# Kernel tuning notes

Hardware: AMD Instinct MI355X
Metric: run time of the kernel (lower is better)

The kernel has to match this reference:

```python
import jax, jax.numpy as jnp
import numpy as np

N_NODES = 50000
N_EDGES = 600000
D = 128
R = 8


def setup_inputs() -> dict:
    key = jax.random.key(0)
    ks = jax.random.split(key, 10)
    return {
        "node_ids": jnp.arange(N_NODES, dtype=jnp.int32),
        "src": jax.random.randint(ks[0], (N_EDGES,), 0, N_NODES, dtype=jnp.int32),
        "dst": jax.random.randint(ks[1], (N_EDGES,), 0, N_NODES, dtype=jnp.int32),
        "etype": jax.random.randint(ks[2], (N_EDGES,), 0, R, dtype=jnp.int32),
        "emb": jax.random.normal(ks[3], (N_NODES, D), dtype=jnp.float32) * 0.02,
        "W1": jax.random.normal(ks[4], (R, D, D), dtype=jnp.float32) * 0.05,
        "Wself1": jax.random.normal(ks[5], (D, D), dtype=jnp.float32) * 0.05,
        "b1": jnp.zeros((D,), dtype=jnp.float32),
        "W2": jax.random.normal(ks[6], (R, D, D), dtype=jnp.float32) * 0.05,
        "Wself2": jax.random.normal(ks[7], (D, D), dtype=jnp.float32) * 0.05,
        "b2": jnp.zeros((D,), dtype=jnp.float32),
    }


def rgcn_layer(h, W, Wself, b, src, dst, etype, n_nodes):
    # relation-wise transform of all node features: [R, N, d_out]
    hr = jnp.einsum('nd,rdo->rno', h, W)
    # per-edge gather of (relation, src) -> message, then scatter-sum to dst
    msgs = hr[etype, src]                                   # [E, d_out]
    agg = jax.ops.segment_sum(msgs, dst, num_segments=n_nodes)
    # self-loop + bias (activation=None, feat_drop=0)
    return agg + h @ Wself + b


def reference(node_ids, src, dst, etype, emb, W1, Wself1, b1, W2, Wself2, b2):
    h0 = emb[node_ids]                                      # embedding lookup over all nodes
    h1 = rgcn_layer(h0, W1, Wself1, b1, src, dst, etype, emb.shape[0])
    h2 = rgcn_layer(h1, W2, Wself2, b2, src, dst, etype, emb.shape[0])
    return h2
```

## Files before the change

kernel.cpp:

```cpp
#include <hip/hip_runtime.h>
#include <hip/hip_bf16.h>

#define NN 50000
#define NE 600000
#define DD 128
#define NR 8
#define NCHUNK ((NN + 255) / 256)

typedef __attribute__((ext_vector_type(8))) short bf16x8;
typedef __attribute__((ext_vector_type(4))) float f32x4;

__device__ __forceinline__ unsigned short f2bf(float f) {
  __hip_bfloat16 h = __float2bfloat16(f);
  return *reinterpret_cast<unsigned short*>(&h);
}
__device__ __forceinline__ unsigned pk2(float lo, float hi) {
  return (unsigned)f2bf(lo) | ((unsigned)f2bf(hi) << 16);
}
__device__ __forceinline__ float bflo(unsigned u) { return __uint_as_float(u << 16); }
__device__ __forceinline__ float bfhi(unsigned u) { return __uint_as_float(u & 0xffff0000u); }

__global__ __launch_bounds__(128) void convw_kernel(
    const float* __restrict__ W1, const float* __restrict__ Ws1,
    const float* __restrict__ W2, const float* __restrict__ Ws2,
    unsigned short* __restrict__ WT)
{
  const int m = blockIdx.y, o = blockIdx.x, d = threadIdx.x;
  const float* src;
  if (m < 8)       src = W1 + (size_t)m * DD * DD;
  else if (m == 8) src = Ws1;
  else if (m < 17) src = W2 + (size_t)(m - 9) * DD * DD;
  else             src = Ws2;
  WT[(size_t)m * DD * DD + o * DD + d] = f2bf(src[(size_t)d * DD + o]);
}

template<int AF32, int OUTF32>
__global__ __launch_bounds__(256) void transform_mfma(
    const void* __restrict__ hin, const int* __restrict__ ids,
    const unsigned short* __restrict__ WT,
    const float* __restrict__ bias,
    unsigned short* __restrict__ hr,
    void* __restrict__ outSelf)
{
  __shared__ __align__(16) char ldsW[DD * DD * 2];

  const int r = blockIdx.y;
  const int rowBase = blockIdx.x * 64;
  const int tid = threadIdx.x;

  {
    const unsigned short* wsrc = WT + (size_t)r * DD * DD;
#pragma unroll
    for (int j = 0; j < 8; ++j) {
      const int i = tid + j * 256;
      const int o = i >> 4, seg = i & 15;
      uint4 v = *reinterpret_cast<const uint4*>(wsrc + o * DD + seg * 8);
      const int dstB = ((o << 8) + (seg << 4)) ^ ((o & 7) << 4);
      *reinterpret_cast<uint4*>(ldsW + dstB) = v;
    }
  }

  const int lane = tid & 63;
  const int w = tid >> 6;
  const int c = lane & 15;
  const int g = lane >> 4;
  const int n = rowBase + w * 16 + c;
  const int nld = (n < NN) ? n : (NN - 1);

  bf16x8 hfrag[4];
  if (AF32) {
    const int srcRow = ids[nld];
    const float* hrow = (const float*)hin + (size_t)srcRow * DD;
#pragma unroll
    for (int ks = 0; ks < 4; ++ks) {
      const float4 x = *reinterpret_cast<const float4*>(hrow + ks * 32 + g * 8);
      const float4 y = *reinterpret_cast<const float4*>(hrow + ks * 32 + g * 8 + 4);
      uint4 u;
      u.x = pk2(x.x, x.y); u.y = pk2(x.z, x.w);
      u.z = pk2(y.x, y.y); u.w = pk2(y.z, y.w);
      hfrag[ks] = *reinterpret_cast<bf16x8*>(&u);
    }
  } else {
    const unsigned short* hrow = (const unsigned short*)hin + (size_t)nld * DD;
#pragma unroll
    for (int ks = 0; ks < 4; ++ks) {
      uint4 u = *reinterpret_cast<const uint4*>(hrow + ks * 32 + g * 8);
      hfrag[ks] = *reinterpret_cast<bf16x8*>(&u);
    }
  }

  __syncthreads();

  f32x4 acc[8];
#pragma unroll
  for (int t = 0; t < 8; ++t) acc[t] = (f32x4){0.f, 0.f, 0.f, 0.f};

#pragma unroll
  for (int ks = 0; ks < 4; ++ks) {
#pragma unroll
    for (int t = 0; t < 8; ++t) {
      const int addr = (((t * 16 + c) << 8) + (ks << 6) + (g << 4)) ^ ((c & 7) << 4);
      bf16x8 a = *reinterpret_cast<const bf16x8*>(ldsW + addr);
      acc[t] = __builtin_amdgcn_mfma_f32_16x16x32_bf16(a, hfrag[ks], acc[t], 0, 0, 0);
    }
  }

  if (n >= NN) return;

  if (r < NR) {
    unsigned short* dst = hr + ((size_t)r * NN + n) * DD;
#pragma unroll
    for (int t = 0; t < 8; ++t) {
      const int o0 = t * 16 + g * 4;
      uint2 u;
      u.x = pk2(acc[t][0], acc[t][1]);
      u.y = pk2(acc[t][2], acc[t][3]);
      *reinterpret_cast<uint2*>(dst + o0) = u;
    }
  } else if (OUTF32) {
    float* dst = (float*)outSelf + (size_t)n * DD;
#pragma unroll
    for (int t = 0; t < 8; ++t) {
      const int o0 = t * 16 + g * 4;
      const float4 bv = *reinterpret_cast<const float4*>(bias + o0);
      float4 o;
      o.x = acc[t][0] + bv.x; o.y = acc[t][1] + bv.y;
      o.z = acc[t][2] + bv.z; o.w = acc[t][3] + bv.w;
      *reinterpret_cast<float4*>(dst + o0) = o;
    }
  } else {
    unsigned short* dst = (unsigned short*)outSelf + (size_t)n * DD;
#pragma unroll
    for (int t = 0; t < 8; ++t) {
      const int o0 = t * 16 + g * 4;
      const float4 bv = *reinterpret_cast<const float4*>(bias + o0);
      uint2 u;
      u.x = pk2(acc[t][0] + bv.x, acc[t][1] + bv.y);
      u.y = pk2(acc[t][2] + bv.z, acc[t][3] + bv.w);
      *reinterpret_cast<uint2*>(dst + o0) = u;
    }
  }
}

__global__ __launch_bounds__(256) void hist_kernel(
    const int* __restrict__ dst, int* __restrict__ deg)
{
  const int e = blockIdx.x * 256 + threadIdx.x;
  if (e < NE) atomicAdd(&deg[dst[e]], 1);
}

__global__ __launch_bounds__(256) void bsum_kernel(
    const int* __restrict__ deg, int* __restrict__ bsum)
{
  __shared__ int tmp[256];
  const int t = threadIdx.x;
  const int i = blockIdx.x * 256 + t;
  tmp[t] = (i < NN) ? deg[i] : 0;
  __syncthreads();
#pragma unroll
  for (int off = 128; off > 0; off >>= 1) {
    if (t < off) tmp[t] += tmp[t + off];
    __syncthreads();
  }
  if (t == 0) bsum[blockIdx.x] = tmp[0];
}

__global__ __launch_bounds__(256) void bscan_kernel(
    const int* __restrict__ bsum, int* __restrict__ bbase)
{
  __shared__ int tmp[256];
  const int t = threadIdx.x;
  const int v = (t < NCHUNK) ? bsum[t] : 0;
  tmp[t] = v;
  __syncthreads();
#pragma unroll
  for (int off = 1; off < 256; off <<= 1) {
    const int x = (t >= off) ? tmp[t - off] : 0;
    __syncthreads();
    tmp[t] += x;
    __syncthreads();
  }
  if (t < NCHUNK) bbase[t] = tmp[t] - v;
}

__global__ __launch_bounds__(256) void expand_kernel(
    int* deg, const int* __restrict__ bbase, int* __restrict__ offsets)
{
  __shared__ int tmp[256];
  const int t = threadIdx.x;
  const int i = blockIdx.x * 256 + t;
  const int v = (i < NN) ? deg[i] : 0;
  tmp[t] = v;
  __syncthreads();
#pragma unroll
  for (int off = 1; off < 256; off <<= 1) {
    const int x = (t >= off) ? tmp[t - off] : 0;
    __syncthreads();
    tmp[t] += x;
    __syncthreads();
  }
  const int base = bbase[blockIdx.x];
  const int excl = base + tmp[t] - v;
  if (i < NN) {
    offsets[i] = excl;
    deg[i] = excl;
    if (i == NN - 1) offsets[NN] = base + tmp[t];
  }
}

__global__ __launch_bounds__(256) void fill_kernel(
    const int* __restrict__ src, const int* __restrict__ dst,
    const int* __restrict__ et, int* __restrict__ cursor,
    int* __restrict__ eidx)
{
  const int e = blockIdx.x * 256 + threadIdx.x;
  if (e < NE) {
    const int pos = atomicAdd(&cursor[dst[e]], 1);
    eidx[pos] = et[e] * NN + src[e];
  }
}

template<int BF16OUT>
__global__ __launch_bounds__(256) void aggregate_kernel(
    const unsigned short* __restrict__ hr,
    const int* __restrict__ offsets, const int* __restrict__ eidx,
    void* __restrict__ outv)
{
  const int node = blockIdx.x * 4 + (threadIdx.x >> 6);
  const int lane = threadIdx.x & 63;
  if (node >= NN) return;
  const int beg = offsets[node];
  const int end = offsets[node + 1];

  float a0 = 0.f, a1 = 0.f;
  int e = beg;
  for (; e + 3 < end; e += 4) {
    const int r0 = eidx[e], r1 = eidx[e + 1], r2 = eidx[e + 2], r3 = eidx[e + 3];
    const unsigned u0 = *reinterpret_cast<const unsigned*>(hr + (size_t)r0 * DD + lane * 2);
    const unsigned u1 = *reinterpret_cast<const unsigned*>(hr + (size_t)r1 * DD + lane * 2);
    const unsigned u2 = *reinterpret_cast<const unsigned*>(hr + (size_t)r2 * DD + lane * 2);
    const unsigned u3 = *reinterpret_cast<const unsigned*>(hr + (size_t)r3 * DD + lane * 2);
    a0 += (bflo(u0) + bflo(u1)) + (bflo(u2) + bflo(u3));
    a1 += (bfhi(u0) + bfhi(u1)) + (bfhi(u2) + bfhi(u3));
  }
  for (; e < end; ++e) {
    const unsigned u0 = *reinterpret_cast<const unsigned*>(hr + (size_t)eidx[e] * DD + lane * 2);
    a0 += bflo(u0);
    a1 += bfhi(u0);
  }

  if (BF16OUT) {
    unsigned* o = reinterpret_cast<unsigned*>((unsigned short*)outv + (size_t)node * DD + lane * 2);
    const unsigned u = *o;
    *o = pk2(bflo(u) + a0, bfhi(u) + a1);
  } else {
    float2* o = reinterpret_cast<float2*>((float*)outv + (size_t)node * DD + lane * 2);
    float2 v = *o;
    v.x += a0; v.y += a1;
    *o = v;
  }
}

extern "C" void kernel_launch(void* const* d_in, const int* in_sizes, int n_in,
                              void* d_out, int out_size, void* d_ws, size_t ws_size,
                              hipStream_t stream) {
  const int*   node_ids = (const int*)d_in[0];
  const int*   src   = (const int*)d_in[1];
  const int*   dst   = (const int*)d_in[2];
  const int*   etype = (const int*)d_in[3];
  const float* emb   = (const float*)d_in[4];
  const float* W1    = (const float*)d_in[5];
  const float* Ws1   = (const float*)d_in[6];
  const float* b1    = (const float*)d_in[7];
  const float* W2    = (const float*)d_in[8];
  const float* Ws2   = (const float*)d_in[9];
  const float* b2    = (const float*)d_in[10];

  char* p = (char*)d_ws;
  unsigned short* hr   = (unsigned short*)p;  p += (size_t)NR * NN * DD * 2;
  unsigned short* h1bf = (unsigned short*)p;  p += (size_t)NN * DD * 2;
  unsigned short* WT   = (unsigned short*)p;  p += (size_t)18 * DD * DD * 2;
  int* offsets         = (int*)p;             p += (size_t)(NN + 1) * 4;
  int* deg             = (int*)p;             p += (size_t)NN * 4;
  int* eidx            = (int*)p;             p += (size_t)NE * 4;
  int* bsum            = (int*)p;             p += 256 * 4;
  int* bbase           = (int*)p;

  const int eb = (NE + 255) / 256;
  dim3 tgrid((NN + 63) / 64, NR + 1);
  const int ab = (NN + 3) / 4;

  convw_kernel<<<dim3(DD, 18), 128, 0, stream>>>(W1, Ws1, W2, Ws2, WT);
  hipMemsetAsync(deg, 0, (size_t)NN * 4, stream);
  hist_kernel<<<eb, 256, 0, stream>>>(dst, deg);
  bsum_kernel<<<NCHUNK, 256, 0, stream>>>(deg, bsum);
  bscan_kernel<<<1, 256, 0, stream>>>(bsum, bbase);
  expand_kernel<<<NCHUNK, 256, 0, stream>>>(deg, bbase, offsets);
  fill_kernel<<<eb, 256, 0, stream>>>(src, dst, etype, deg, eidx);

  transform_mfma<1, 0><<<tgrid, 256, 0, stream>>>(emb, node_ids, WT, b1, hr, h1bf);
  aggregate_kernel<1><<<ab, 256, 0, stream>>>(hr, offsets, eidx, h1bf);
  transform_mfma<0, 1><<<tgrid, 256, 0, stream>>>(h1bf, nullptr, WT + (size_t)9 * DD * DD, b2, hr, (float*)d_out);
  aggregate_kernel<0><<<ab, 256, 0, stream>>>(hr, offsets, eidx, (float*)d_out);
}
```

Measured before the change: 265.3 us.

## Loop over relations in one block with double-buffered LDS weight prefetch

Each transform block now handles all nine weight matrices for its 64 rows instead of launching one block per relation. The input row fragment is loaded and converted once and reused across relations. The next weight matrix is prefetched into registers and written to a second LDS buffer while the current one feeds the MFMAs. This removes repeated loads and bf16 conversion of the activations, but it doubles LDS use to 64KB per block and shrinks the grid ninefold, which may lower occupancy and parallelism.

After: 272.0 us. 2.5% more time.

```diff
diff --git a/kernel.cpp b/kernel.cpp
--- a/kernel.cpp
+++ b/kernel.cpp
@@ -42,24 +42,10 @@
     unsigned short* __restrict__ hr,
     void* __restrict__ outSelf)
 {
-  __shared__ __align__(16) char ldsW[DD * DD * 2];
-
-  const int r = blockIdx.y;
+  __shared__ __align__(16) char ldsW[2][DD * DD * 2];
+
+  const int tid = threadIdx.x;
   const int rowBase = blockIdx.x * 64;
-  const int tid = threadIdx.x;
-
-  {
-    const unsigned short* wsrc = WT + (size_t)r * DD * DD;
-#pragma unroll
-    for (int j = 0; j < 8; ++j) {
-      const int i = tid + j * 256;
-      const int o = i >> 4, seg = i & 15;
-      uint4 v = *reinterpret_cast<const uint4*>(wsrc + o * DD + seg * 8);
-      const int dstB = ((o << 8) + (seg << 4)) ^ ((o & 7) << 4);
-      *reinterpret_cast<uint4*>(ldsW + dstB) = v;
-    }
-  }
-
   const int lane = tid & 63;
   const int w = tid >> 6;
   const int c = lane & 15;
@@ -89,55 +75,87 @@
     }
   }
 
-  __syncthreads();
-
-  f32x4 acc[8];
-#pragma unroll
-  for (int t = 0; t < 8; ++t) acc[t] = (f32x4){0.f, 0.f, 0.f, 0.f};
-
-#pragma unroll
-  for (int ks = 0; ks < 4; ++ks) {
-#pragma unroll
-    for (int t = 0; t < 8; ++t) {
-      const int addr = (((t * 16 + c) << 8) + (ks << 6) + (g << 4)) ^ ((c & 7) << 4);
-      bf16x8 a = *reinterpret_cast<const bf16x8*>(ldsW + addr);
-      acc[t] = __builtin_amdgcn_mfma_f32_16x16x32_bf16(a, hfrag[ks], acc[t], 0, 0, 0);
-    }
-  }
-
-  if (n >= NN) return;
-
-  if (r < NR) {
-    unsigned short* dst = hr + ((size_t)r * NN + n) * DD;
-#pragma unroll
-    for (int t = 0; t < 8; ++t) {
-      const int o0 = t * 16 + g * 4;
-      uint2 u;
-      u.x = pk2(acc[t][0], acc[t][1]);
-      u.y = pk2(acc[t][2], acc[t][3]);
-      *reinterpret_cast<uint2*>(dst + o0) = u;
-    }
-  } else if (OUTF32) {
-    float* dst = (float*)outSelf + (size_t)n * DD;
-#pragma unroll
-    for (int t = 0; t < 8; ++t) {
-      const int o0 = t * 16 + g * 4;
-      const float4 bv = *reinterpret_cast<const float4*>(bias + o0);
-      float4 o;
-      o.x = acc[t][0] + bv.x; o.y = acc[t][1] + bv.y;
-      o.z = acc[t][2] + bv.z; o.w = acc[t][3] + bv.w;
-      *reinterpret_cast<float4*>(dst + o0) = o;
-    }
-  } else {
-    unsigned short* dst = (unsigned short*)outSelf + (size_t)n * DD;
-#pragma unroll
-    for (int t = 0; t < 8; ++t) {
-      const int o0 = t * 16 + g * 4;
-      const float4 bv = *reinterpret_cast<const float4*>(bias + o0);
-      uint2 u;
-      u.x = pk2(acc[t][0] + bv.x, acc[t][1] + bv.y);
-      u.y = pk2(acc[t][2] + bv.z, acc[t][3] + bv.w);
-      *reinterpret_cast<uint2*>(dst + o0) = u;
+  int srcOff[8];
+#pragma unroll
+  for (int j = 0; j < 8; ++j) {
+    const int dstB = (tid + j * 256) * 16;
+    const int srcB = dstB ^ (((dstB >> 8) & 7) << 4);
+    srcOff[j] = srcB >> 1;
+  }
+
+  uint4 wreg[8];
+#pragma unroll
+  for (int j = 0; j < 8; ++j)
+    wreg[j] = *reinterpret_cast<const uint4*>(WT + srcOff[j]);
+#pragma unroll
+  for (int j = 0; j < 8; ++j)
+    *reinterpret_cast<uint4*>(ldsW[0] + (tid + j * 256) * 16) = wreg[j];
+
+  for (int r = 0; r < NR + 1; ++r) {
+    __syncthreads();
+    const char* buf = ldsW[r & 1];
+
+    if (r < NR) {
+      const unsigned short* wnext = WT + (size_t)(r + 1) * DD * DD;
+#pragma unroll
+      for (int j = 0; j < 8; ++j)
+        wreg[j] = *reinterpret_cast<const uint4*>(wnext + srcOff[j]);
+    }
+
+    f32x4 acc[8];
+#pragma unroll
+    for (int t = 0; t < 8; ++t) acc[t] = (f32x4){0.f, 0.f, 0.f, 0.f};
+#pragma unroll
+    for (int ks = 0; ks < 4; ++ks) {
+#pragma unroll
+      for (int t = 0; t < 8; ++t) {
+        const int addr = (((t * 16 + c) << 8) + (ks << 6) + (g << 4)) ^ ((c & 7) << 4);
+        bf16x8 a = *reinterpret_cast<const bf16x8*>(buf + addr);
+        acc[t] = __builtin_amdgcn_mfma_f32_16x16x32_bf16(a, hfrag[ks], acc[t], 0, 0, 0);
+      }
+    }
+
+    if (n < NN) {
+      if (r < NR) {
+        unsigned short* dst = hr + ((size_t)r * NN + n) * DD;
+#pragma unroll
+        for (int t = 0; t < 8; ++t) {
+          const int o0 = t * 16 + g * 4;
+          uint2 u;
+          u.x = pk2(acc[t][0], acc[t][1]);
+          u.y = pk2(acc[t][2], acc[t][3]);
+          *reinterpret_cast<uint2*>(dst + o0) = u;
+        }
+      } else if (OUTF32) {
+        float* dst = (float*)outSelf + (size_t)n * DD;
+#pragma unroll
+        for (int t = 0; t < 8; ++t) {
+          const int o0 = t * 16 + g * 4;
+          const float4 bv = *reinterpret_cast<const float4*>(bias + o0);
+          float4 o;
+          o.x = acc[t][0] + bv.x; o.y = acc[t][1] + bv.y;
+          o.z = acc[t][2] + bv.z; o.w = acc[t][3] + bv.w;
+          *reinterpret_cast<float4*>(dst + o0) = o;
+        }
+      } else {
+        unsigned short* dst = (unsigned short*)outSelf + (size_t)n * DD;
+#pragma unroll
+        for (int t = 0; t < 8; ++t) {
+          const int o0 = t * 16 + g * 4;
+          const float4 bv = *reinterpret_cast<const float4*>(bias + o0);
+          uint2 u;
+          u.x = pk2(acc[t][0] + bv.x, acc[t][1] + bv.y);
+          u.y = pk2(acc[t][2] + bv.z, acc[t][3] + bv.w);
+          *reinterpret_cast<uint2*>(dst + o0) = u;
+        }
+      }
+    }
+
+    if (r < NR) {
+      char* nbuf = ldsW[(r & 1) ^ 1];
+#pragma unroll
+      for (int j = 0; j < 8; ++j)
+        *reinterpret_cast<uint4*>(nbuf + (tid + j * 256) * 16) = wreg[j];
     }
   }
 }
@@ -287,7 +305,7 @@
   int* bbase           = (int*)p;
 
   const int eb = (NE + 255) / 256;
-  dim3 tgrid((NN + 63) / 64, NR + 1);
+  const int tb = (NN + 63) / 64;
   const int ab = (NN + 3) / 4;
 
   convw_kernel<<<dim3(DD, 18), 128, 0, stream>>>(W1, Ws1, W2, Ws2, WT);
@@ -298,8 +316,8 @@
   expand_kernel<<<NCHUNK, 256, 0, stream>>>(deg, bbase, offsets);
   fill_kernel<<<eb, 256, 0, stream>>>(src, dst, etype, deg, eidx);
 
-  transform_mfma<1, 0><<<tgrid, 256, 0, stream>>>(emb, node_ids, WT, b1, hr, h1bf);
+  transform_mfma<1, 0><<<tb, 256, 0, stream>>>(emb, node_ids, WT, b1, hr, h1bf);
   aggregate_kernel<1><<<ab, 256, 0, stream>>>(hr, offsets, eidx, h1bf);
-  transform_mfma<0, 1><<<tgrid, 256, 0, stream>>>(h1bf, nullptr, WT + (size_t)9 * DD * DD, b2, hr, (float*)d_out);
+  transform_mfma<0, 1><<<tb, 256, 0, stream>>>(h1bf, nullptr, WT + (size_t)9 * DD * DD, b2, hr, (float*)d_out);
   aggregate_kernel<0><<<ab, 256, 0, stream>>>(hr, offsets, eidx, (float*)d_out);
 }
```
